# Optimization experiments

Hardware: AMD Instinct MI355X
Metric: run time of the kernel (lower is better)

## Reference

```python
import jax, jax.numpy as jnp
from jax import lax
import numpy as np

B, S, G = 64, 200, 8
CHAR_V, GAZ_V = 8000, 100000
D_CHAR, D_GAZ, H = 128, 128, 512
N_LABEL = 20
N_TAG = N_LABEL + 2  # CRF adds START (N_TAG-2) and STOP (N_TAG-1)


def setup_inputs() -> dict:
    key = jax.random.key(0)
    ks = jax.random.split(key, 16)
    lengths = jax.random.randint(ks[0], (B,), S // 2, S + 1)
    pos = jnp.arange(S)[None, :]
    mask = pos < lengths[:, None]
    char_inputs = jax.random.randint(ks[1], (B, S), 0, CHAR_V)
    gaz_ids = jax.random.randint(ks[2], (B, S, G), 0, GAZ_V)
    cnt = jax.random.randint(ks[3], (B, S), 1, G + 1)
    gaz_mask = (jnp.arange(G)[None, None, :] < cnt[..., None]).astype(jnp.int32)
    rev_gaz_ids = jax.random.randint(ks[4], (B, S, G), 0, GAZ_V)
    rcnt = jax.random.randint(ks[5], (B, S), 1, G + 1)
    rev_gaz_mask = (jnp.arange(G)[None, None, :] < rcnt[..., None]).astype(jnp.int32)
    sc = 0.1
    D_in = D_CHAR + D_GAZ
    return dict(
        char_inputs=char_inputs, lengths=lengths, mask=mask,
        gaz_ids=gaz_ids, gaz_mask=gaz_mask,
        rev_gaz_ids=rev_gaz_ids, rev_gaz_mask=rev_gaz_mask,
        char_table=jax.random.normal(ks[6], (CHAR_V, D_CHAR)) * sc,
        gaz_table=jax.random.normal(ks[7], (GAZ_V, D_GAZ)) * sc,
        w_ih_f=jax.random.normal(ks[8], (4 * H, D_in)) * sc,
        w_hh_f=jax.random.normal(ks[9], (4 * H, H)) * sc,
        b_f=jnp.zeros((4 * H,), jnp.float32),
        w_ih_b=jax.random.normal(ks[10], (4 * H, D_in)) * sc,
        w_hh_b=jax.random.normal(ks[11], (4 * H, H)) * sc,
        b_b=jnp.zeros((4 * H,), jnp.float32),
        W_out=jax.random.normal(ks[12], (2 * H, N_TAG)) * sc,
        b_out=jnp.zeros((N_TAG,), jnp.float32),
        transitions=jax.random.normal(ks[13], (N_TAG, N_TAG)) * sc,
    )


def rev_pad(x, lengths):
    # reverse each sequence within its valid length (reverse_padded_sequence)
    b, s = x.shape[0], x.shape[1]
    pos = jnp.arange(s)[None, :]
    idx = jnp.where(pos < lengths[:, None], lengths[:, None] - 1 - pos, pos)
    idx = idx.reshape((b, s) + (1,) * (x.ndim - 2))
    return jnp.take_along_axis(x, jnp.broadcast_to(idx, x.shape), axis=1)


def gaz_embed(table, ids, m):
    # masked mean over the G candidate gaz words per char (Gaz_Embed, type=1)
    e = table[ids]                                   # [B,S,G,D]
    mf = m.astype(e.dtype)[..., None]
    return (e * mf).sum(2) / jnp.maximum(mf.sum(2), 1.0)


def lstm(x, w_ih, w_hh, b):
    # x: [B,S,D]; torch gate order i,f,g,o
    h0 = jnp.zeros((x.shape[0], H), x.dtype)

    def step(carry, xt):
        h, c = carry
        g = xt @ w_ih.T + h @ w_hh.T + b
        i, f, gg, o = jnp.split(g, 4, axis=-1)
        c = jax.nn.sigmoid(f) * c + jax.nn.sigmoid(i) * jnp.tanh(gg)
        h = jax.nn.sigmoid(o) * jnp.tanh(c)
        return (h, c), h

    _, hs = lax.scan(step, (h0, h0), x.transpose(1, 0, 2))
    return hs.transpose(1, 0, 2)                     # [B,S,H]


def emissions_fn(char_inputs, lengths, gaz_ids, gaz_mask, rev_gaz_ids, rev_gaz_mask,
                 char_table, gaz_table, w_ih_f, w_hh_f, b_f, w_ih_b, w_hh_b, b_b,
                 W_out, b_out):
    char_embs = char_table[char_inputs]              # [B,S,Dc]
    rev_char_embs = rev_pad(char_embs, lengths)
    g_f = gaz_embed(gaz_table, gaz_ids, gaz_mask)
    g_b = gaz_embed(gaz_table, rev_pad(rev_gaz_ids, lengths), rev_pad(rev_gaz_mask, lengths))
    fwd_in = jnp.concatenate([char_embs, g_f], axis=-1)
    bwd_in = jnp.concatenate([rev_char_embs, g_b], axis=-1)
    h_f = lstm(fwd_in, w_ih_f, w_hh_f, b_f)
    h_b = rev_pad(lstm(bwd_in, w_ih_b, w_hh_b, b_b), lengths)
    lstm_outs = jnp.concatenate([h_f, h_b], axis=-1)  # [B,S,2H]
    return lstm_outs @ W_out + b_out                  # [B,S,N_TAG]


def viterbi(emissions, mask, transitions):
    # transitions[prev, next]; START=N_TAG-2, STOP=N_TAG-1
    n = emissions.shape[-1]
    start, stop = n - 2, n - 1
    init = emissions[:, 0] + transitions[start][None, :]     # [B,n]
    ident = jnp.arange(n, dtype=jnp.int32)[None, :]

    def vstep(part, inp):
        emit_t, m_t = inp                                    # [B,n], [B]
        cand = part[:, :, None] + transitions[None] + emit_t[:, None, :]
        new = cand.max(axis=1)
        bp = cand.argmax(axis=1).astype(jnp.int32)
        part = jnp.where(m_t[:, None], new, part)
        bp = jnp.where(m_t[:, None], bp, ident)              # identity bp on pad
        return part, bp

    part, bps = lax.scan(vstep, init,
                         (emissions[:, 1:].transpose(1, 0, 2), mask[:, 1:].T))
    last_tag = (part + transitions[:, stop][None, :]).argmax(-1).astype(jnp.int32)

    def btstep(tag, bp):
        prev = jnp.take_along_axis(bp, tag[:, None], axis=1)[:, 0]
        return prev, prev

    _, prev_tags = lax.scan(btstep, last_tag, bps, reverse=True)  # [S-1,B]
    tags = jnp.concatenate([prev_tags.T, last_tag[:, None]], axis=1)
    return tags * mask.astype(tags.dtype)


def reference(char_inputs, lengths, mask, gaz_ids, gaz_mask, rev_gaz_ids, rev_gaz_mask,
              char_table, gaz_table, w_ih_f, w_hh_f, b_f, w_ih_b, w_hh_b, b_b,
              W_out, b_out, transitions):
    emissions = emissions_fn(char_inputs, lengths, gaz_ids, gaz_mask,
                             rev_gaz_ids, rev_gaz_mask, char_table, gaz_table,
                             w_ih_f, w_hh_f, b_f, w_ih_b, w_hh_b, b_b, W_out, b_out)
    return viterbi(emissions, mask, transitions)
```

## Files before the change

### kernel.cpp

```cpp
#include <hip/hip_runtime.h>
#include <math.h>

#define S_LEN 200
#define BATCH 64
#define HID   512
#define NTAG  22
#define TCH   40
#define MC    (TCH*BATCH)

typedef unsigned short u16;
typedef unsigned int   u32;

__device__ __forceinline__ float bf2f(u16 u){
  union { u32 ui; float f; } v; v.ui = ((u32)u) << 16; return v.f;
}

__global__ void k_detect(const u32* __restrict__ w, int* __restrict__ flag){
  __shared__ int cnt;
  if (threadIdx.x == 0) cnt = 0;
  __syncthreads();
  int hits = 0;
  for (int i = threadIdx.x; i < 16384; i += 256){
    u32 e = (w[i] & 0x7F80u);
    if (e >= 0x3800u && e <= 0x4080u) hits++;
  }
  atomicAdd(&cnt, hits);
  __syncthreads();
  if (threadIdx.x == 0) *flag = (cnt > 8192) ? 1 : 0;
}

__global__ void k_cvt_f(const void* __restrict__ src, float* __restrict__ dst,
                        int n, const int* __restrict__ flag){
  int i = blockIdx.x*blockDim.x + threadIdx.x;
  if (i >= n) return;
  if (*flag) dst[i] = bf2f(((const u16*)src)[i]);
  else       dst[i] = ((const float*)src)[i];
}

__global__ void k_cvt_wt(const void* __restrict__ src, float* __restrict__ dst,
                         const int* __restrict__ flag){
  int i = blockIdx.x*blockDim.x + threadIdx.x;
  if (i >= 1024*24) return;
  int k = i / 24, tag = i % 24;
  float v = 0.f;
  if (tag < NTAG){
    v = (*flag) ? bf2f(((const u16*)src)[k*NTAG + tag])
                : ((const float*)src)[k*NTAG + tag];
  }
  int half = k >> 9, kk = k & 511;
  dst[((size_t)half*512 + kk)*24 + tag] = v;
}

__global__ void k_zero(float* __restrict__ p, int n){
  int i = blockIdx.x*blockDim.x + threadIdx.x;
  if (i < n) p[i] = 0.f;
}

__global__ __launch_bounds__(128)
void k_build(const int* __restrict__ ci, const int* __restrict__ lengths,
             const int* __restrict__ gid, const int* __restrict__ gm,
             const int* __restrict__ rgid, const int* __restrict__ rgm,
             const void* __restrict__ ctab, const void* __restrict__ gtab,
             const int* __restrict__ flag,
             float* __restrict__ fin, float* __restrict__ bin)
{
  int bs = blockIdx.x;
  int b = bs / S_LEN, s = bs % S_LEN;
  int d = threadIdx.x;
  int isbf = *flag;
  int len = lengths[b];
  int sb = (s < len) ? (len - 1 - s) : s;
  size_t orow = ((size_t)s*BATCH + b)*256;

  {
    int cid = ci[bs];
    float cv = isbf ? bf2f(((const u16*)ctab)[(size_t)cid*128 + d])
                    : ((const float*)ctab)[(size_t)cid*128 + d];
    fin[orow + d] = cv;
    const int* gg = gid + (size_t)bs*8;
    const int* mm = gm  + (size_t)bs*8;
    float sum = 0.f, cntf = 0.f;
    for (int g = 0; g < 8; ++g){
      float m = (float)mm[g];
      int gw = gg[g];
      float gv = isbf ? bf2f(((const u16*)gtab)[(size_t)gw*128 + d])
                      : ((const float*)gtab)[(size_t)gw*128 + d];
      sum += m * gv; cntf += m;
    }
    fin[orow + 128 + d] = sum / fmaxf(cntf, 1.f);
  }
  {
    int bsr = b*S_LEN + sb;
    int cid = ci[bsr];
    float cv = isbf ? bf2f(((const u16*)ctab)[(size_t)cid*128 + d])
                    : ((const float*)ctab)[(size_t)cid*128 + d];
    bin[orow + d] = cv;
    const int* gg = rgid + (size_t)bsr*8;
    const int* mm = rgm  + (size_t)bsr*8;
    float sum = 0.f, cntf = 0.f;
    for (int g = 0; g < 8; ++g){
      float m = (float)mm[g];
      int gw = gg[g];
      float gv = isbf ? bf2f(((const u16*)gtab)[(size_t)gw*128 + d])
                      : ((const float*)gtab)[(size_t)gw*128 + d];
      sum += m * gv; cntf += m;
    }
    bin[orow + 128 + d] = sum / fmaxf(cntf, 1.f);
  }
}

__global__ __launch_bounds__(256)
void k_gemm_ih(const float* __restrict__ Af, const float* __restrict__ Ab,
               const float* __restrict__ wih,
               const float* __restrict__ bias,
               float* __restrict__ gxc,
               int t0)
{
  const int dir = blockIdx.z;
  const float* A = (dir ? Ab : Af) + (size_t)t0*BATCH*256;
  const float* W = wih + (size_t)dir*2048*256;
  const float* bi = bias + (size_t)dir*2048;
  float* C = gxc + (size_t)dir*2048*MC;
  const int m0 = blockIdx.y * 128;
  const int n0 = blockIdx.x * 128;
  const int tid = threadIdx.x;

  __shared__ float As[32][132];
  __shared__ float Ws[32][132];

  const int lrow = tid >> 3;
  const int lk   = (tid & 7) * 4;

  const int tx = tid & 15;
  const int ty = tid >> 4;

  float acc[8][8] = {};

  for (int k0 = 0; k0 < 256; k0 += 32){
    #pragma unroll
    for (int q = 0; q < 4; ++q){
      const int row = lrow + q*32;
      float4 a = *(const float4*)(A + (size_t)(m0+row)*256 + k0 + lk);
      float4 w = *(const float4*)(W + (size_t)(n0+row)*256 + k0 + lk);
      As[lk+0][row]=a.x; As[lk+1][row]=a.y; As[lk+2][row]=a.z; As[lk+3][row]=a.w;
      Ws[lk+0][row]=w.x; Ws[lk+1][row]=w.y; Ws[lk+2][row]=w.z; Ws[lk+3][row]=w.w;
    }
    __syncthreads();
    #pragma unroll 8
    for (int kk = 0; kk < 32; ++kk){
      float4 a0 = *(const float4*)(&As[kk][ty*8]);
      float4 a1 = *(const float4*)(&As[kk][ty*8+4]);
      float4 w0 = *(const float4*)(&Ws[kk][tx*8]);
      float4 w1 = *(const float4*)(&Ws[kk][tx*8+4]);
      float am[8] = {a0.x,a0.y,a0.z,a0.w,a1.x,a1.y,a1.z,a1.w};
      float wn[8] = {w0.x,w0.y,w0.z,w0.w,w1.x,w1.y,w1.z,w1.w};
      #pragma unroll
      for (int i = 0; i < 8; ++i)
        #pragma unroll
        for (int jj = 0; jj < 8; ++jj)
          acc[i][jj] += am[i]*wn[jj];
    }
    __syncthreads();
  }

  #pragma unroll
  for (int jj = 0; jj < 8; ++jj){
    const int n = n0 + tx*8 + jj;
    const float bj = bi[n];
    #pragma unroll
    for (int i = 0; i < 8; i += 4){
      float4 o = make_float4(acc[i][jj]+bj, acc[i+1][jj]+bj,
                             acc[i+2][jj]+bj, acc[i+3][jj]+bj);
      *(float4*)(C + (size_t)n*MC + m0 + ty*8 + i) = o;
    }
  }
}

__global__ __launch_bounds__(512)
void k_step(const float* __restrict__ whh,
            const float* __restrict__ gxc,
            float* __restrict__ hbuf,
            float* __restrict__ cbuf,
            float* __restrict__ hseq,
            int t, int tc)
{
  const int dir = blockIdx.y;
  const int hrow_base = blockIdx.x * 4;
  const int tid = threadIdx.x;
  const int b = tid & 63;
  const int uw = __builtin_amdgcn_readfirstlane(tid >> 6);
  const int uk0 = uw * 64;

  __shared__ float part[8*16*64];

  const float* hprev = hbuf + (size_t)(dir*2 + (t&1))*HID*BATCH;
  float* hnext       = hbuf + (size_t)(dir*2 + ((t+1)&1))*HID*BATCH;
  const float* whhd  = whh + (size_t)dir*2048*512;

  float hv[64];
  #pragma unroll
  for (int j = 0; j < 64; ++j)
    hv[j] = hprev[(size_t)(uk0 + j)*BATCH + b];

  float acc[16];
  #pragma unroll
  for (int r = 0; r < 16; ++r) acc[r] = 0.f;

  #pragma unroll
  for (int r = 0; r < 16; ++r){
    const int row_glob = (r >> 2)*512 + hrow_base + (r & 3);
    const float* wr = whhd + (size_t)row_glob*512 + uk0;
    #pragma unroll
    for (int j = 0; j < 64; ++j)
      acc[r] += wr[j] * hv[j];
  }

  #pragma unroll
  for (int r = 0; r < 16; ++r)
    part[(uw*16 + r)*64 + b] = acc[r];
  __syncthreads();

  if (tid < 256){
    const int hr = tid >> 6;
    const int bb = tid & 63;
    const int hrow = hrow_base + hr;
    float g4[4];
    #pragma unroll
    for (int g = 0; g < 4; ++g){
      const int r = g*4 + hr;
      float s = 0.f;
      #pragma unroll
      for (int ww = 0; ww < 8; ++ww)
        s += part[(ww*16 + r)*64 + bb];
      g4[g] = s;
    }
    const float* gxb = gxc + (size_t)dir*2048*MC + (size_t)tc*BATCH + bb;
    float gi = g4[0] + gxb[(size_t)(   0 + hrow)*MC];
    float gf = g4[1] + gxb[(size_t)( 512 + hrow)*MC];
    float gg = g4[2] + gxb[(size_t)(1024 + hrow)*MC];
    float go = g4[3] + gxb[(size_t)(1536 + hrow)*MC];
    float si = 1.f/(1.f+expf(-gi));
    float sf = 1.f/(1.f+expf(-gf));
    float so = 1.f/(1.f+expf(-go));
    size_t ci_ = ((size_t)dir*HID + hrow)*BATCH + bb;
    float c = cbuf[ci_];
    c = sf*c + si*tanhf(gg);
    float h = so*tanhf(c);
    cbuf[ci_] = c;
    hnext[(size_t)hrow*BATCH + bb] = h;
    hseq[(((size_t)dir*S_LEN + t)*HID + hrow)*BATCH + bb] = h;
  }
}

__global__ __launch_bounds__(256)
void k_emis(const float* __restrict__ hseq, const int* __restrict__ lengths,
            const float* __restrict__ wpad,
            const float* __restrict__ bout,
            float* __restrict__ emisF, float* __restrict__ emisB)
{
  const int t = blockIdx.x;
  const int dir = blockIdx.y;
  const int tid = threadIdx.x;
  const int b = tid & 63;
  const int utg = __builtin_amdgcn_readfirstlane(tid >> 6);

  __shared__ float hl[64*64];

  const float* hsrc = hseq + ((size_t)(dir*S_LEN + t)*HID)*BATCH;
  const float* wbase = wpad + (size_t)dir*512*24 + utg*6;

  float acc[6] = {0.f,0.f,0.f,0.f,0.f,0.f};

  for (int c = 0; c < 8; ++c){
    const float4* s4 = (const float4*)(hsrc + (size_t)c*64*64);
    float4* d4 = (float4*)hl;
    #pragma unroll
    for (int q = 0; q < 4; ++q) d4[q*256 + tid] = s4[q*256 + tid];
    __syncthreads();
    const float* wrow = wbase + (size_t)c*64*24;
    #pragma unroll 4
    for (int k = 0; k < 64; ++k){
      float hval = hl[k*64 + b];
      #pragma unroll
      for (int i = 0; i < 6; ++i) acc[i] += hval * wrow[k*24 + i];
    }
    __syncthreads();
  }

  const int len = lengths[b];
  const int pos = dir ? ((t < len) ? (len - 1 - t) : t) : t;
  float* dst = (dir ? emisB : emisF) + ((size_t)b*S_LEN + pos)*NTAG;
  #pragma unroll
  for (int i = 0; i < 6; ++i){
    int tag = utg*6 + i;
    if (tag < NTAG) dst[tag] = acc[i] + (dir ? 0.f : bout[tag]);
  }
}

__global__ __launch_bounds__(64)
void k_viterbi(const float* __restrict__ emisF, const float* __restrict__ emisB,
               const int* __restrict__ lengths,
               const float* __restrict__ trans, int* __restrict__ out)
{
  const int b = blockIdx.x;
  const int j = threadIdx.x;
  __shared__ float part[2][NTAG];
  __shared__ unsigned char bp[(S_LEN-1)*NTAG];
  const int len = lengths[b];
  const float* ef = emisF + (size_t)b*S_LEN*NTAG;
  const float* eb = emisB + (size_t)b*S_LEN*NTAG;

  float trr[NTAG];
  if (j < NTAG){
    #pragma unroll
    for (int i = 0; i < NTAG; ++i) trr[i] = trans[i*NTAG + j];
    part[0][j] = ef[j] + eb[j] + trans[(NTAG-2)*NTAG + j];
  }
  __syncthreads();

  for (int t = 1; t < S_LEN; ++t){
    const int cur = (t-1) & 1, nxt = t & 1;
    if (j < NTAG){
      float v[NTAG];
      #pragma unroll
      for (int i = 0; i < NTAG; ++i) v[i] = part[cur][i] + trr[i];
      float m1[11]; int x1[11];
      #pragma unroll
      for (int i = 0; i < 11; ++i){
        const bool g = v[2*i+1] > v[2*i];
        m1[i] = g ? v[2*i+1] : v[2*i];
        x1[i] = g ? 2*i+1 : 2*i;
      }
      float m2[6]; int x2[6];
      #pragma unroll
      for (int i = 0; i < 5; ++i){
        const bool g = m1[2*i+1] > m1[2*i];
        m2[i] = g ? m1[2*i+1] : m1[2*i];
        x2[i] = g ? x1[2*i+1] : x1[2*i];
      }
      m2[5] = m1[10]; x2[5] = x1[10];
      float m3[3]; int x3[3];
      #pragma unroll
      for (int i = 0; i < 3; ++i){
        const bool g = m2[2*i+1] > m2[2*i];
        m3[i] = g ? m2[2*i+1] : m2[2*i];
        x3[i] = g ? x2[2*i+1] : x2[2*i];
      }
      const bool g01 = m3[1] > m3[0];
      float mm = g01 ? m3[1] : m3[0];
      int   xx = g01 ? x3[1] : x3[0];
      const bool g2 = m3[2] > mm;
      mm = g2 ? m3[2] : mm;
      xx = g2 ? x3[2] : xx;

      const float e = ef[t*NTAG + j] + eb[t*NTAG + j];
      if (t < len){ part[nxt][j] = mm + e; bp[(t-1)*NTAG + j] = (unsigned char)xx; }
      else        { part[nxt][j] = part[cur][j]; bp[(t-1)*NTAG + j] = (unsigned char)j; }
    }
    __syncthreads();
  }

  if (j == 0){
    const int fin = (S_LEN-1) & 1;
    float best = -3.4e38f; int tag = 0;
    for (int i = 0; i < NTAG; ++i){
      float vv = part[fin][i] + trans[i*NTAG + (NTAG-1)];
      if (vv > best){ best = vv; tag = i; }
    }
    out[b*S_LEN + S_LEN-1] = (S_LEN-1 < len) ? tag : 0;
    for (int t = S_LEN-2; t >= 0; --t){
      tag = bp[t*NTAG + tag];
      out[b*S_LEN + t] = (t < len) ? tag : 0;
    }
  }
}

extern "C" void kernel_launch(void* const* d_in, const int* in_sizes, int n_in,
                              void* d_out, int out_size, void* d_ws, size_t ws_size,
                              hipStream_t stream)
{
  (void)in_sizes; (void)n_in; (void)out_size; (void)ws_size;
  const int* char_inputs  = (const int*)d_in[0];
  const int* lengths      = (const int*)d_in[1];
  const int* gaz_ids      = (const int*)d_in[3];
  const int* gaz_mask     = (const int*)d_in[4];
  const int* rev_gaz_ids  = (const int*)d_in[5];
  const int* rev_gaz_mask = (const int*)d_in[6];
  const void* char_table  = d_in[7];
  const void* gaz_table   = d_in[8];
  const void* w_ih_f = d_in[9];
  const void* w_hh_f = d_in[10];
  const void* b_f    = d_in[11];
  const void* w_ih_b = d_in[12];
  const void* w_hh_b = d_in[13];
  const void* b_b    = d_in[14];
  const void* W_out  = d_in[15];
  const void* b_out  = d_in[16];
  const void* trans  = d_in[17];

  char* ws = (char*)d_ws;
  size_t off = 0;
  auto alloc = [&](size_t bytes)->char*{
    char* p = ws + off; off = (off + bytes + 255) & ~(size_t)255; return p;
  };
  int*   flag   = (int*)  alloc(256);
  float* whh32  = (float*)alloc(2ull*2048*512*4);
  float* wih32  = (float*)alloc(2ull*2048*256*4);
  float* bias32 = (float*)alloc(2ull*2048*4);
  float* wpad   = (float*)alloc(2ull*512*24*4);
  float* bout32 = (float*)alloc(22ull*4);
  float* trans32= (float*)alloc(484ull*4);
  float* fwd_in = (float*)alloc(12800ull*256*4);
  float* bwd_in = (float*)alloc(12800ull*256*4);
  float* gxc    = (float*)alloc(2ull*2048*MC*4);
  float* hbuf   = (float*)alloc(2ull*2*512*64*4);
  float* cbuf   = (float*)alloc(2ull*512*64*4);
  float* hseq   = (float*)alloc(2ull*200*512*64*4);
  float* emisF  = (float*)alloc(12800ull*22*4);
  float* emisB  = (float*)alloc(12800ull*22*4);

  k_detect<<<1,256,0,stream>>>((const u32*)char_table, flag);
  k_cvt_f<<<4096,256,0,stream>>>(w_hh_f, whh32,           1048576, flag);
  k_cvt_f<<<4096,256,0,stream>>>(w_hh_b, whh32 + 1048576, 1048576, flag);
  k_cvt_f<<<2048,256,0,stream>>>(w_ih_f, wih32,            524288, flag);
  k_cvt_f<<<2048,256,0,stream>>>(w_ih_b, wih32 + 524288,   524288, flag);
  k_cvt_f<<<8,256,0,stream>>>(b_f, bias32,        2048, flag);
  k_cvt_f<<<8,256,0,stream>>>(b_b, bias32 + 2048, 2048, flag);
  k_cvt_wt<<<96,256,0,stream>>>(W_out, wpad, flag);
  k_cvt_f<<<1,256,0,stream>>>(b_out, bout32, 22, flag);
  k_cvt_f<<<2,256,0,stream>>>(trans, trans32, 484, flag);

  k_build<<<12800,128,0,stream>>>(char_inputs, lengths, gaz_ids, gaz_mask,
                                  rev_gaz_ids, rev_gaz_mask, char_table, gaz_table,
                                  flag, fwd_in, bwd_in);

  k_zero<<<768,256,0,stream>>>(hbuf, 2*2*512*64 + 2*512*64);

  for (int t0 = 0; t0 < S_LEN; t0 += TCH){
    k_gemm_ih<<<dim3(16,MC/128,2),256,0,stream>>>(fwd_in, bwd_in, wih32, bias32,
                                                  gxc, t0);
    for (int tc = 0; tc < TCH; ++tc)
      k_step<<<dim3(128,2),512,0,stream>>>(whh32, gxc, hbuf, cbuf, hseq, t0+tc, tc);
  }

  k_emis<<<dim3(S_LEN,2),256,0,stream>>>(hseq, lengths, wpad, bout32, emisF, emisB);
  k_viterbi<<<64,64,0,stream>>>(emisF, emisB, lengths, trans32, (int*)d_out);
}
```

Measured before the change: 2.805 ms.

## Stage recurrent weights in LDS and run Viterbi with wave-level lane reads

In the LSTM step kernel, each block's 16 recurrent-weight rows are loaded cooperatively into shared memory with float4 loads, and the matvec then reads them as vectorized LDS loads instead of per-thread strided global reads. The Viterbi kernel now precomputes the summed emissions into shared memory and keeps the partition vector in registers, broadcasting it with readlane, so the per-timestep shared-memory round trip and block barrier are gone. The costs are extra LDS usage in the step kernel, which may reduce occupancy, and an added barrier after the weight staging.

```diff
diff --git a/kernel.cpp b/kernel.cpp
--- a/kernel.cpp
+++ b/kernel.cpp
@@ -13,6 +13,10 @@
 
 __device__ __forceinline__ float bf2f(u16 u){
   union { u32 ui; float f; } v; v.ui = ((u32)u) << 16; return v.f;
+}
+
+__device__ __forceinline__ float rdlane(float x, int lane){
+  return __int_as_float(__builtin_amdgcn_readlane(__float_as_int(x), lane));
 }
 
 __global__ void k_detect(const u32* __restrict__ w, int* __restrict__ flag){
@@ -191,28 +195,38 @@
   const int uw = __builtin_amdgcn_readfirstlane(tid >> 6);
   const int uk0 = uw * 64;
 
+  __shared__ float wl[4*4*512];
   __shared__ float part[8*16*64];
 
   const float* hprev = hbuf + (size_t)(dir*2 + (t&1))*HID*BATCH;
   float* hnext       = hbuf + (size_t)(dir*2 + ((t+1)&1))*HID*BATCH;
   const float* whhd  = whh + (size_t)dir*2048*512;
 
+  #pragma unroll
+  for (int g = 0; g < 4; ++g){
+    float4 v = *(const float4*)(whhd + ((size_t)g*512 + hrow_base)*512 + tid*4);
+    *(float4*)(&wl[g*2048 + tid*4]) = v;
+  }
+
   float hv[64];
   #pragma unroll
   for (int j = 0; j < 64; ++j)
     hv[j] = hprev[(size_t)(uk0 + j)*BATCH + b];
 
+  __syncthreads();
+
   float acc[16];
   #pragma unroll
   for (int r = 0; r < 16; ++r) acc[r] = 0.f;
 
   #pragma unroll
   for (int r = 0; r < 16; ++r){
-    const int row_glob = (r >> 2)*512 + hrow_base + (r & 3);
-    const float* wr = whhd + (size_t)row_glob*512 + uk0;
-    #pragma unroll
-    for (int j = 0; j < 64; ++j)
-      acc[r] += wr[j] * hv[j];
+    const float* wr = &wl[(r >> 2)*2048 + (r & 3)*512 + uk0];
+    #pragma unroll
+    for (int j4 = 0; j4 < 16; ++j4){
+      float4 w = *(const float4*)(wr + j4*4);
+      acc[r] += w.x*hv[4*j4] + w.y*hv[4*j4+1] + w.z*hv[4*j4+2] + w.w*hv[4*j4+3];
+    }
   }
 
   #pragma unroll
@@ -304,67 +318,68 @@
 {
   const int b = blockIdx.x;
   const int j = threadIdx.x;
-  __shared__ float part[2][NTAG];
+  __shared__ float esum[S_LEN*NTAG];
   __shared__ unsigned char bp[(S_LEN-1)*NTAG];
-  const int len = lengths[b];
+
   const float* ef = emisF + (size_t)b*S_LEN*NTAG;
   const float* eb = emisB + (size_t)b*S_LEN*NTAG;
-
+  for (int i = j; i < S_LEN*NTAG; i += 64) esum[i] = ef[i] + eb[i];
+
+  const int len = lengths[b];
   float trr[NTAG];
-  if (j < NTAG){
-    #pragma unroll
-    for (int i = 0; i < NTAG; ++i) trr[i] = trans[i*NTAG + j];
-    part[0][j] = ef[j] + eb[j] + trans[(NTAG-2)*NTAG + j];
-  }
-  __syncthreads();
+  #pragma unroll
+  for (int i = 0; i < NTAG; ++i)
+    trr[i] = (j < NTAG) ? trans[i*NTAG + j] : 0.f;
+  __syncthreads();
+
+  float p = (j < NTAG) ? (esum[j] + trans[(NTAG-2)*NTAG + j]) : -3.4e38f;
 
   for (int t = 1; t < S_LEN; ++t){
-    const int cur = (t-1) & 1, nxt = t & 1;
-    if (j < NTAG){
-      float v[NTAG];
-      #pragma unroll
-      for (int i = 0; i < NTAG; ++i) v[i] = part[cur][i] + trr[i];
-      float m1[11]; int x1[11];
-      #pragma unroll
-      for (int i = 0; i < 11; ++i){
-        const bool g = v[2*i+1] > v[2*i];
-        m1[i] = g ? v[2*i+1] : v[2*i];
-        x1[i] = g ? 2*i+1 : 2*i;
-      }
-      float m2[6]; int x2[6];
-      #pragma unroll
-      for (int i = 0; i < 5; ++i){
-        const bool g = m1[2*i+1] > m1[2*i];
-        m2[i] = g ? m1[2*i+1] : m1[2*i];
-        x2[i] = g ? x1[2*i+1] : x1[2*i];
-      }
-      m2[5] = m1[10]; x2[5] = x1[10];
-      float m3[3]; int x3[3];
-      #pragma unroll
-      for (int i = 0; i < 3; ++i){
-        const bool g = m2[2*i+1] > m2[2*i];
-        m3[i] = g ? m2[2*i+1] : m2[2*i];
-        x3[i] = g ? x2[2*i+1] : x2[2*i];
-      }
-      const bool g01 = m3[1] > m3[0];
-      float mm = g01 ? m3[1] : m3[0];
-      int   xx = g01 ? x3[1] : x3[0];
-      const bool g2 = m3[2] > mm;
-      mm = g2 ? m3[2] : mm;
-      xx = g2 ? x3[2] : xx;
-
-      const float e = ef[t*NTAG + j] + eb[t*NTAG + j];
-      if (t < len){ part[nxt][j] = mm + e; bp[(t-1)*NTAG + j] = (unsigned char)xx; }
-      else        { part[nxt][j] = part[cur][j]; bp[(t-1)*NTAG + j] = (unsigned char)j; }
-    }
-    __syncthreads();
-  }
+    float v[NTAG];
+    #pragma unroll
+    for (int i = 0; i < NTAG; ++i)
+      v[i] = rdlane(p, i) + trr[i];
+    float m1[11]; int x1[11];
+    #pragma unroll
+    for (int i = 0; i < 11; ++i){
+      const bool g = v[2*i+1] > v[2*i];
+      m1[i] = g ? v[2*i+1] : v[2*i];
+      x1[i] = g ? 2*i+1 : 2*i;
+    }
+    float m2[6]; int x2[6];
+    #pragma unroll
+    for (int i = 0; i < 5; ++i){
+      const bool g = m1[2*i+1] > m1[2*i];
+      m2[i] = g ? m1[2*i+1] : m1[2*i];
+      x2[i] = g ? x1[2*i+1] : x1[2*i];
+    }
+    m2[5] = m1[10]; x2[5] = x1[10];
+    float m3[3]; int x3[3];
+    #pragma unroll
+    for (int i = 0; i < 3; ++i){
+      const bool g = m2[2*i+1] > m2[2*i];
+      m3[i] = g ? m2[2*i+1] : m2[2*i];
+      x3[i] = g ? x2[2*i+1] : x2[2*i];
+    }
+    const bool g01 = m3[1] > m3[0];
+    float mm = g01 ? m3[1] : m3[0];
+    int   xx = g01 ? x3[1] : x3[0];
+    const bool g2 = m3[2] > mm;
+    mm = g2 ? m3[2] : mm;
+    xx = g2 ? x3[2] : xx;
+
+    const float e = esum[t*NTAG + j];
+    if (j < NTAG)
+      bp[(t-1)*NTAG + j] = (unsigned char)((t < len) ? xx : j);
+    p = (t < len && j < NTAG) ? (mm + e) : p;
+  }
+  __syncthreads();
 
   if (j == 0){
-    const int fin = (S_LEN-1) & 1;
     float best = -3.4e38f; int tag = 0;
+    #pragma unroll
     for (int i = 0; i < NTAG; ++i){
-      float vv = part[fin][i] + trans[i*NTAG + (NTAG-1)];
+      float vv = rdlane(p, i) + trans[i*NTAG + (NTAG-1)];
       if (vv > best){ best = vv; tag = i; }
     }
     out[b*S_LEN + S_LEN-1] = (S_LEN-1 < len) ? tag : 0;
```

Measured after the change: 2.747 ms. -2.1%, faster.
